# Performance work log

Measured on AMD Instinct MI355X. Metric: run time of the kernel, lower is better.

Reference implementation:

```python
import jax, jax.numpy as jnp
import numpy as np

D_MODEL = 1024
NUM_HEADS = 16
DEPTH = D_MODEL // NUM_HEADS


def setup_inputs() -> dict:
    key = jax.random.key(0)
    ks = jax.random.split(key, 9)
    s = 1.0 / np.sqrt(D_MODEL)
    x = jax.random.normal(ks[0], (2, 2048, D_MODEL), dtype=jnp.float32)
    def lin(kw, kb):
        W = jax.random.uniform(kw, (D_MODEL, D_MODEL), jnp.float32, -s, s)
        b = jax.random.uniform(kb, (D_MODEL,), jnp.float32, -s, s)
        return W, b
    Wq, bq = lin(ks[1], ks[2])
    Wk, bk = lin(ks[3], ks[4])
    Wv, bv = lin(ks[5], ks[6])
    Wo, bo = lin(ks[7], ks[8])
    return {"x": x, "Wq": Wq, "bq": bq, "Wk": Wk, "bk": bk,
            "Wv": Wv, "bv": bv, "Wo": Wo, "bo": bo}


def reference(x, Wq, bq, Wk, bk, Wv, bv, Wo, bo):
    B, T, _ = x.shape
    # projections; weights stored as [in, out] (torch Linear applies x @ W.T; here W is already [in,out])
    def split_heads(y):
        return y.reshape(B, T, NUM_HEADS, DEPTH).transpose(0, 2, 1, 3)  # [B,H,T,D]
    Q = split_heads(x @ Wq + bq)
    K = split_heads(x @ Wk + bk)
    V = split_heads(x @ Wv + bv)
    scale = 1.0 / jnp.sqrt(jnp.asarray(DEPTH, dtype=x.dtype))
    scores = jnp.einsum('bhqd,bhkd->bhqk', Q, K) * scale  # [B,H,T,T]
    attn = jax.nn.softmax(scores, axis=-1)
    out = jnp.einsum('bhqk,bhkd->bhqd', attn, V)  # [B,H,T,D]
    out = out.transpose(0, 2, 1, 3).reshape(B, T, D_MODEL)
    return out @ Wo + bo
```

## Files before the change

kernel.cpp:

```cpp
#include <hip/hip_runtime.h>
#include <hip/hip_bf16.h>

typedef unsigned short ushort_t;
typedef short s8v __attribute__((ext_vector_type(8)));
typedef float f4v __attribute__((ext_vector_type(4)));

#define DM 1024
#define TT 2048
#define NH 16
#define DH 64
#define QSCALE 0.18033688011112042f

__device__ __forceinline__ ushort_t f2bf(float f) {
  union { float f; unsigned u; } v; v.f = f;
  unsigned u = v.u;
  return (ushort_t)((u + 0x7fffu + ((u >> 16) & 1u)) >> 16);
}

__device__ __forceinline__ unsigned pk2bf(float a, float b) {
  union { __hip_bfloat162 h; unsigned u; } v;
  v.h = __float22bfloat162_rn(float2{a, b});
  return v.u;
}

__device__ __forceinline__ void gll16(const void* g, const void* l) {
  __builtin_amdgcn_global_load_lds(
      (const __attribute__((address_space(1))) unsigned int*)g,
      (__attribute__((address_space(3))) unsigned int*)l, 16, 0, 0);
}

__global__ __launch_bounds__(256) void wtrans4_kernel(const float* __restrict__ W0,
                                                      const float* __restrict__ W1,
                                                      const float* __restrict__ W2,
                                                      const float* __restrict__ W3,
                                                      ushort_t* __restrict__ dst) {
  __shared__ float tile[32][33];
  const int z = blockIdx.z;
  const float* W = z == 0 ? W0 : (z == 1 ? W1 : (z == 2 ? W2 : W3));
  ushort_t* Wt = dst + (size_t)z * DM * DM;
  int tx = threadIdx.x & 31, ty = threadIdx.x >> 5;
  int n0 = blockIdx.x * 32, k0 = blockIdx.y * 32;
#pragma unroll
  for (int i = 0; i < 4; i++)
    tile[ty + i * 8][tx] = W[(size_t)(k0 + ty + i * 8) * DM + n0 + tx];
  __syncthreads();
#pragma unroll
  for (int i = 0; i < 4; i++)
    Wt[(size_t)(n0 + ty + i * 8) * DM + k0 + tx] = f2bf(tile[tx][ty + i * 8]);
}

__global__ __launch_bounds__(256) void xconv_kernel(const float* __restrict__ x,
                                                    ushort_t* __restrict__ xb) {
  int i = blockIdx.x * 256 + threadIdx.x;
  const float4* p = (const float4*)x + (size_t)i * 2;
  float4 a = p[0], b = p[1];
  union { ushort_t s[8]; uint4 u; } r;
  r.s[0] = f2bf(a.x); r.s[1] = f2bf(a.y); r.s[2] = f2bf(a.z); r.s[3] = f2bf(a.w);
  r.s[4] = f2bf(b.x); r.s[5] = f2bf(b.y); r.s[6] = f2bf(b.z); r.s[7] = f2bf(b.w);
  *((uint4*)xb + i) = r.u;
}

__global__ __launch_bounds__(256) void vtrans_kernel(const ushort_t* __restrict__ V,
                                                     ushort_t* __restrict__ Vt) {
  __shared__ ushort_t Ls[64][72];
  const int t = threadIdx.x;
  const int t0 = blockIdx.x * 64, bh = blockIdx.y;
  const ushort_t* Vb = V + (size_t)bh * TT * DH;
  ushort_t* Vtb = Vt + (size_t)bh * DH * TT;
#pragma unroll
  for (int c = t; c < 512; c += 256) {
    int tt = c & 63, dch = c >> 6;
    union { uint4 u; ushort_t s[8]; } uu;
    uu.u = *(const uint4*)&Vb[(size_t)(t0 + tt) * DH + dch * 8];
#pragma unroll
    for (int i = 0; i < 8; i++) Ls[dch * 8 + i][tt] = uu.s[i];
  }
  __syncthreads();
#pragma unroll
  for (int c = t; c < 512; c += 256) {
    int d = c >> 3, tch = c & 7;
    uint4 u = *(const uint4*)&Ls[d][tch * 8];
    *(uint4*)&Vtb[(size_t)d * TT + t0 + tch * 8] = u;
  }
}

__global__ __launch_bounds__(256) void gemm_bt(
    const ushort_t* __restrict__ A, const ushort_t* __restrict__ Bt, int mode,
    const float* __restrict__ bias0, const float* __restrict__ bias1,
    const float* __restrict__ bias2,
    ushort_t* __restrict__ qo, ushort_t* __restrict__ ko, ushort_t* __restrict__ vo,
    float* __restrict__ co) {
  __shared__ __align__(16) ushort_t Asm[128 * 32];
  __shared__ __align__(16) ushort_t Bsm[128 * 32];
  const int m0 = blockIdx.x * 128, n0 = blockIdx.y * 128;
  const int t = threadIdx.x, lane = t & 63;
  const int wid = t >> 6, wr = wid >> 1, wc = wid & 1;
  const ushort_t* Ab = A + (size_t)m0 * DM;
  const ushort_t* Bb = Bt + (size_t)n0 * DM;

  f4v zero = {0.f, 0.f, 0.f, 0.f};
  f4v acc[4][4];
#pragma unroll
  for (int i = 0; i < 4; i++)
#pragma unroll
    for (int j = 0; j < 4; j++) acc[i][j] = zero;

  const int r0 = t >> 2;
  const int r1 = (t + 256) >> 2;
  const int k8a = (t & 3) * 8;
  const int rr = lane & 15, kk = (lane >> 4) * 8;

  for (int k0 = 0; k0 < DM; k0 += 32) {
    __syncthreads();
    gll16(Ab + (size_t)r0 * DM + k0 + k8a, &Asm[t * 8]);
    gll16(Ab + (size_t)r1 * DM + k0 + k8a, &Asm[(t + 256) * 8]);
    gll16(Bb + (size_t)r0 * DM + k0 + k8a, &Bsm[t * 8]);
    gll16(Bb + (size_t)r1 * DM + k0 + k8a, &Bsm[(t + 256) * 8]);
    asm volatile("s_waitcnt vmcnt(0)" ::: "memory");
    __syncthreads();

    s8v af[4], bf_[4];
#pragma unroll
    for (int mt = 0; mt < 4; mt++)
      af[mt] = *(const s8v*)&Asm[(wr * 64 + mt * 16 + rr) * 32 + kk];
#pragma unroll
    for (int nt = 0; nt < 4; nt++)
      bf_[nt] = *(const s8v*)&Bsm[(wc * 64 + nt * 16 + rr) * 32 + kk];
#pragma unroll
    for (int mt = 0; mt < 4; mt++)
#pragma unroll
      for (int nt = 0; nt < 4; nt++)
        acc[mt][nt] =
            __builtin_amdgcn_mfma_f32_16x16x32_bf16(af[mt], bf_[nt], acc[mt][nt], 0, 0, 0);
  }

  const int col_l = lane & 15, row_q = (lane >> 4) * 4;
  if (mode == 0) {
    const int qkv = n0 >> 10;
    const float* bias = qkv == 0 ? bias0 : (qkv == 1 ? bias1 : bias2);
    ushort_t* dst = qkv == 0 ? qo : (qkv == 1 ? ko : vo);
    const float sc = qkv == 0 ? QSCALE : 1.0f;
    const int nb = n0 & 1023;
#pragma unroll
    for (int nt = 0; nt < 4; nt++) {
      int gc = nb + wc * 64 + nt * 16 + col_l;
      float bv_ = bias[gc];
      int hh = gc >> 6, d = gc & 63;
#pragma unroll
      for (int mt = 0; mt < 4; mt++) {
#pragma unroll
        for (int j = 0; j < 4; j++) {
          int r = m0 + wr * 64 + mt * 16 + row_q + j;
          int bb = r >> 11, tt_ = r & 2047;
          dst[(((size_t)(bb * NH + hh)) * TT + tt_) * DH + d] = f2bf((acc[mt][nt][j] + bv_) * sc);
        }
      }
    }
  } else {
#pragma unroll
    for (int nt = 0; nt < 4; nt++) {
      int gc = n0 + wc * 64 + nt * 16 + col_l;
      float bv_ = bias0[gc];
#pragma unroll
      for (int mt = 0; mt < 4; mt++) {
#pragma unroll
        for (int j = 0; j < 4; j++) {
          int r = m0 + wr * 64 + mt * 16 + row_q + j;
          co[(size_t)r * DM + gc] = acc[mt][nt][j] + bv_;
        }
      }
    }
  }
}

__global__ __launch_bounds__(256) void attn_kernel(const ushort_t* __restrict__ Q,
                                                   const ushort_t* __restrict__ K,
                                                   const ushort_t* __restrict__ Vt,
                                                   ushort_t* __restrict__ O) {
  __shared__ __align__(16) ushort_t Ksm[64 * 64];
  __shared__ __align__(16) ushort_t Vsm[64 * 64];
  __shared__ __align__(16) ushort_t Psm[4][32 * 64];

  const int qt = blockIdx.x;
  const int bh = blockIdx.y;
  const int b = bh >> 4, h = bh & 15;
  const int t = threadIdx.x, lane = t & 63, wid = t >> 6;
  const ushort_t* Qb = Q + ((size_t)bh * TT + qt * 128) * DH;
  const ushort_t* Kb = K + (size_t)bh * TT * DH;
  const ushort_t* Vb = Vt + (size_t)bh * DH * TT;
  const int rr = lane & 15, quad = lane >> 4;
  const int rx = rr & 7;

  s8v qf[2][2];
#pragma unroll
  for (int mt = 0; mt < 2; mt++)
#pragma unroll
    for (int kh = 0; kh < 2; kh++)
      qf[mt][kh] = *(const s8v*)&Qb[(size_t)(wid * 32 + mt * 16 + rr) * DH + kh * 32 + quad * 8];

  f4v zero = {0.f, 0.f, 0.f, 0.f};
  f4v oacc[2][4];
  float mreg[2], lreg[2];
#pragma unroll
  for (int mt = 0; mt < 2; mt++) {
#pragma unroll
    for (int dt = 0; dt < 4; dt++) oacc[mt][dt] = zero;
    mreg[mt] = -1e30f;
    lreg[mt] = 0.f;
  }

  ushort_t* Pw = &Psm[wid][0];

  for (int kv0 = 0; kv0 < TT; kv0 += 64) {
    __syncthreads();
#pragma unroll
    for (int c = t; c < 512; c += 256) {
      int row = c >> 3;
      int sch = ((c & 7) ^ (row & 7)) * 8;
      gll16(&Kb[(size_t)(kv0 + row) * DH + sch], &Ksm[c * 8]);
      gll16(&Vb[(size_t)row * TT + kv0 + sch], &Vsm[c * 8]);
    }
    asm volatile("s_waitcnt vmcnt(0)" ::: "memory");
    __syncthreads();

    f4v st[2][4];
#pragma unroll
    for (int mt = 0; mt < 2; mt++)
#pragma unroll
      for (int ct = 0; ct < 4; ct++) st[mt][ct] = zero;
    __builtin_amdgcn_s_setprio(1);
#pragma unroll
    for (int ct = 0; ct < 4; ct++) {
      int key = ct * 16 + rr;
#pragma unroll
      for (int kh = 0; kh < 2; kh++) {
        s8v kf = *(const s8v*)&Ksm[key * 64 + (((kh * 4 + quad) ^ (key & 7)) << 3)];
#pragma unroll
        for (int mt = 0; mt < 2; mt++)
          st[mt][ct] = __builtin_amdgcn_mfma_f32_16x16x32_bf16(kf, qf[mt][kh], st[mt][ct], 0, 0, 0);
      }
    }
    __builtin_amdgcn_s_setprio(0);

#pragma unroll
    for (int mt = 0; mt < 2; mt++) {
      float a0 = fmaxf(fmaxf(st[mt][0][0], st[mt][0][1]), fmaxf(st[mt][0][2], st[mt][0][3]));
      float a1 = fmaxf(fmaxf(st[mt][1][0], st[mt][1][1]), fmaxf(st[mt][1][2], st[mt][1][3]));
      float a2 = fmaxf(fmaxf(st[mt][2][0], st[mt][2][1]), fmaxf(st[mt][2][2], st[mt][2][3]));
      float a3 = fmaxf(fmaxf(st[mt][3][0], st[mt][3][1]), fmaxf(st[mt][3][2], st[mt][3][3]));
      float pmax = fmaxf(fmaxf(a0, a1), fmaxf(a2, a3));
      pmax = fmaxf(pmax, __shfl_xor(pmax, 16, 64));
      pmax = fmaxf(pmax, __shfl_xor(pmax, 32, 64));
      float mold = mreg[mt];
      float mnew = fmaxf(mold, pmax);
      float corr = __builtin_amdgcn_exp2f(mold - mnew);
      mreg[mt] = mnew;
      float ps = 0.f;
#pragma unroll
      for (int ct = 0; ct < 4; ct++) {
#pragma unroll
        for (int j = 0; j < 4; j++) {
          float p = __builtin_amdgcn_exp2f(st[mt][ct][j] - mnew);
          st[mt][ct][j] = p;
          ps += p;
        }
      }
      ps += __shfl_xor(ps, 16, 64);
      ps += __shfl_xor(ps, 32, 64);
      lreg[mt] = lreg[mt] * corr + ps;
#pragma unroll
      for (int j = 0; j < 4; j++) {
        float cb = __shfl(corr, quad * 4 + j, 64);
#pragma unroll
        for (int dt = 0; dt < 4; dt++) oacc[mt][dt][j] *= cb;
      }
    }

#pragma unroll
    for (int mt = 0; mt < 2; mt++) {
#pragma unroll
      for (int ct = 0; ct < 4; ct++) {
        uint2 w;
        w.x = pk2bf(st[mt][ct][0], st[mt][ct][1]);
        w.y = pk2bf(st[mt][ct][2], st[mt][ct][3]);
        int chunk = 2 * ct + (quad >> 1);
        int idx = (mt * 16 + rr) * 64 + ((chunk ^ rx) << 3) + ((quad & 1) << 2);
        *(uint2*)&Pw[idx] = w;
      }
    }
    asm volatile("s_waitcnt lgkmcnt(0)" ::: "memory");
    __builtin_amdgcn_sched_barrier(0);

    __builtin_amdgcn_s_setprio(1);
#pragma unroll
    for (int mt = 0; mt < 2; mt++) {
#pragma unroll
      for (int kh2 = 0; kh2 < 2; kh2++) {
        s8v pa = *(const s8v*)&Pw[(mt * 16 + rr) * 64 + (((kh2 * 4 + quad) ^ rx) << 3)];
#pragma unroll
        for (int dt = 0; dt < 4; dt++) {
          int d = dt * 16 + rr;
          s8v vf = *(const s8v*)&Vsm[d * 64 + (((kh2 * 4 + quad) ^ rx) << 3)];
          oacc[mt][dt] = __builtin_amdgcn_mfma_f32_16x16x32_bf16(pa, vf, oacc[mt][dt], 0, 0, 0);
        }
      }
    }
    __builtin_amdgcn_s_setprio(0);
  }

#pragma unroll
  for (int mt = 0; mt < 2; mt++) {
    float linv = 1.0f / lreg[mt];
#pragma unroll
    for (int j = 0; j < 4; j++) {
      float lb = __shfl(linv, quad * 4 + j, 64);
      int row = qt * 128 + wid * 32 + mt * 16 + quad * 4 + j;
#pragma unroll
      for (int dt = 0; dt < 4; dt++) {
        int d = dt * 16 + rr;
        O[((size_t)(b * TT + row)) * DM + h * DH + d] = f2bf(oacc[mt][dt][j] * lb);
      }
    }
  }
}

extern "C" void kernel_launch(void* const* d_in, const int* in_sizes, int n_in,
                              void* d_out, int out_size, void* d_ws, size_t ws_size,
                              hipStream_t stream) {
  const float* x = (const float*)d_in[0];
  const float* Wq = (const float*)d_in[1];
  const float* bq = (const float*)d_in[2];
  const float* Wk = (const float*)d_in[3];
  const float* bk = (const float*)d_in[4];
  const float* Wv = (const float*)d_in[5];
  const float* bv = (const float*)d_in[6];
  const float* Wo = (const float*)d_in[7];
  const float* bo = (const float*)d_in[8];
  float* out = (float*)d_out;

  char* ws = (char*)d_ws;
  ushort_t* xb = (ushort_t*)(ws);
  ushort_t* wqkv = (ushort_t*)(ws + (8ull << 20));
  ushort_t* wot = (ushort_t*)(ws + (14ull << 20));
  ushort_t* Qb = (ushort_t*)(ws + (16ull << 20));
  ushort_t* Kb = (ushort_t*)(ws + (24ull << 20));
  ushort_t* Vb = (ushort_t*)(ws + (32ull << 20));
  ushort_t* Vtb = xb;
  ushort_t* Ob = Vb;

  dim3 tb(256);
  wtrans4_kernel<<<dim3(32, 32, 4), tb, 0, stream>>>(Wq, Wk, Wv, Wo, wqkv);
  xconv_kernel<<<dim3(2048), tb, 0, stream>>>(x, xb);
  gemm_bt<<<dim3(32, 24), tb, 0, stream>>>(xb, wqkv, 0, bq, bk, bv, Qb, Kb, Vb, nullptr);
  vtrans_kernel<<<dim3(32, 32), tb, 0, stream>>>(Vb, Vtb);
  attn_kernel<<<dim3(16, 32), tb, 0, stream>>>(Qb, Kb, Vtb, Ob);
  gemm_bt<<<dim3(32, 8), tb, 0, stream>>>(Ob, wot, 1, bo, nullptr, nullptr, nullptr, nullptr,
                                          nullptr, out);
}
```

Before: 240.3 us.

## Write V transposed from QKV GEMM, shrink attention tiles, add lazy softmax rescale

The QKV projection epilogue now writes V directly in [bh, d, t] layout, which removes the separate V transpose kernel and its extra memory round trip. The attention kernel uses 64-query blocks with one 16-row tile per wave, giving twice as many blocks and lower register use under a 4-waves occupancy hint. Blocks are remapped so that blocks sharing a head land on the same XCD for K/V cache reuse. Online softmax skips the rescale of the accumulator when the new max exceeds the old by no more than 8 (log2 units). In exchange, the V stores are strided, and each K/V tile now feeds less MFMA work per load.

```diff
diff --git a/kernel.cpp b/kernel.cpp
--- a/kernel.cpp
+++ b/kernel.cpp
@@ -58,30 +58,6 @@
   r.s[0] = f2bf(a.x); r.s[1] = f2bf(a.y); r.s[2] = f2bf(a.z); r.s[3] = f2bf(a.w);
   r.s[4] = f2bf(b.x); r.s[5] = f2bf(b.y); r.s[6] = f2bf(b.z); r.s[7] = f2bf(b.w);
   *((uint4*)xb + i) = r.u;
-}
-
-__global__ __launch_bounds__(256) void vtrans_kernel(const ushort_t* __restrict__ V,
-                                                     ushort_t* __restrict__ Vt) {
-  __shared__ ushort_t Ls[64][72];
-  const int t = threadIdx.x;
-  const int t0 = blockIdx.x * 64, bh = blockIdx.y;
-  const ushort_t* Vb = V + (size_t)bh * TT * DH;
-  ushort_t* Vtb = Vt + (size_t)bh * DH * TT;
-#pragma unroll
-  for (int c = t; c < 512; c += 256) {
-    int tt = c & 63, dch = c >> 6;
-    union { uint4 u; ushort_t s[8]; } uu;
-    uu.u = *(const uint4*)&Vb[(size_t)(t0 + tt) * DH + dch * 8];
-#pragma unroll
-    for (int i = 0; i < 8; i++) Ls[dch * 8 + i][tt] = uu.s[i];
-  }
-  __syncthreads();
-#pragma unroll
-  for (int c = t; c < 512; c += 256) {
-    int d = c >> 3, tch = c & 7;
-    uint4 u = *(const uint4*)&Ls[d][tch * 8];
-    *(uint4*)&Vtb[(size_t)d * TT + t0 + tch * 8] = u;
-  }
 }
 
 __global__ __launch_bounds__(256) void gemm_bt(
@@ -152,7 +128,13 @@
         for (int j = 0; j < 4; j++) {
           int r = m0 + wr * 64 + mt * 16 + row_q + j;
           int bb = r >> 11, tt_ = r & 2047;
-          dst[(((size_t)(bb * NH + hh)) * TT + tt_) * DH + d] = f2bf((acc[mt][nt][j] + bv_) * sc);
+          int bhh = bb * NH + hh;
+          ushort_t val = f2bf((acc[mt][nt][j] + bv_) * sc);
+          if (qkv == 2) {
+            dst[((size_t)bhh * DH + d) * TT + tt_] = val;
+          } else {
+            dst[((size_t)bhh * TT + tt_) * DH + d] = val;
+          }
         }
       }
     }
@@ -173,41 +155,37 @@
   }
 }
 
-__global__ __launch_bounds__(256) void attn_kernel(const ushort_t* __restrict__ Q,
-                                                   const ushort_t* __restrict__ K,
-                                                   const ushort_t* __restrict__ Vt,
-                                                   ushort_t* __restrict__ O) {
+__global__ __launch_bounds__(256, 4) void attn_kernel(const ushort_t* __restrict__ Q,
+                                                      const ushort_t* __restrict__ K,
+                                                      const ushort_t* __restrict__ Vt,
+                                                      ushort_t* __restrict__ O) {
   __shared__ __align__(16) ushort_t Ksm[64 * 64];
   __shared__ __align__(16) ushort_t Vsm[64 * 64];
-  __shared__ __align__(16) ushort_t Psm[4][32 * 64];
-
-  const int qt = blockIdx.x;
-  const int bh = blockIdx.y;
+  __shared__ __align__(16) ushort_t Psm[4][16 * 64];
+
+  const int b_lin = blockIdx.x + (blockIdx.y << 5);
+  const int xcd = b_lin & 7, n = b_lin >> 3;
+  const int bh = (xcd << 2) | (n >> 5);
+  const int qt = n & 31;
   const int b = bh >> 4, h = bh & 15;
   const int t = threadIdx.x, lane = t & 63, wid = t >> 6;
-  const ushort_t* Qb = Q + ((size_t)bh * TT + qt * 128) * DH;
+  const ushort_t* Qb = Q + ((size_t)bh * TT + qt * 64) * DH;
   const ushort_t* Kb = K + (size_t)bh * TT * DH;
   const ushort_t* Vb = Vt + (size_t)bh * DH * TT;
   const int rr = lane & 15, quad = lane >> 4;
   const int rx = rr & 7;
 
-  s8v qf[2][2];
-#pragma unroll
-  for (int mt = 0; mt < 2; mt++)
-#pragma unroll
-    for (int kh = 0; kh < 2; kh++)
-      qf[mt][kh] = *(const s8v*)&Qb[(size_t)(wid * 32 + mt * 16 + rr) * DH + kh * 32 + quad * 8];
+  s8v qf[2];
+#pragma unroll
+  for (int kh = 0; kh < 2; kh++)
+    qf[kh] = *(const s8v*)&Qb[(size_t)(wid * 16 + rr) * DH + kh * 32 + quad * 8];
 
   f4v zero = {0.f, 0.f, 0.f, 0.f};
-  f4v oacc[2][4];
-  float mreg[2], lreg[2];
-#pragma unroll
-  for (int mt = 0; mt < 2; mt++) {
-#pragma unroll
-    for (int dt = 0; dt < 4; dt++) oacc[mt][dt] = zero;
-    mreg[mt] = -1e30f;
-    lreg[mt] = 0.f;
-  }
+  f4v oacc[4];
+  float mreg = -1e30f;
+  float lreg = 0.f;
+#pragma unroll
+  for (int dt = 0; dt < 4; dt++) oacc[dt] = zero;
 
   ushort_t* Pw = &Psm[wid][0];
 
@@ -223,11 +201,9 @@
     asm volatile("s_waitcnt vmcnt(0)" ::: "memory");
     __syncthreads();
 
-    f4v st[2][4];
-#pragma unroll
-    for (int mt = 0; mt < 2; mt++)
-#pragma unroll
-      for (int ct = 0; ct < 4; ct++) st[mt][ct] = zero;
+    f4v st[4];
+#pragma unroll
+    for (int ct = 0; ct < 4; ct++) st[ct] = zero;
     __builtin_amdgcn_s_setprio(1);
 #pragma unroll
     for (int ct = 0; ct < 4; ct++) {
@@ -235,91 +211,84 @@
 #pragma unroll
       for (int kh = 0; kh < 2; kh++) {
         s8v kf = *(const s8v*)&Ksm[key * 64 + (((kh * 4 + quad) ^ (key & 7)) << 3)];
-#pragma unroll
-        for (int mt = 0; mt < 2; mt++)
-          st[mt][ct] = __builtin_amdgcn_mfma_f32_16x16x32_bf16(kf, qf[mt][kh], st[mt][ct], 0, 0, 0);
+        st[ct] = __builtin_amdgcn_mfma_f32_16x16x32_bf16(kf, qf[kh], st[ct], 0, 0, 0);
       }
     }
     __builtin_amdgcn_s_setprio(0);
 
-#pragma unroll
-    for (int mt = 0; mt < 2; mt++) {
-      float a0 = fmaxf(fmaxf(st[mt][0][0], st[mt][0][1]), fmaxf(st[mt][0][2], st[mt][0][3]));
-      float a1 = fmaxf(fmaxf(st[mt][1][0], st[mt][1][1]), fmaxf(st[mt][1][2], st[mt][1][3]));
-      float a2 = fmaxf(fmaxf(st[mt][2][0], st[mt][2][1]), fmaxf(st[mt][2][2], st[mt][2][3]));
-      float a3 = fmaxf(fmaxf(st[mt][3][0], st[mt][3][1]), fmaxf(st[mt][3][2], st[mt][3][3]));
-      float pmax = fmaxf(fmaxf(a0, a1), fmaxf(a2, a3));
-      pmax = fmaxf(pmax, __shfl_xor(pmax, 16, 64));
-      pmax = fmaxf(pmax, __shfl_xor(pmax, 32, 64));
-      float mold = mreg[mt];
-      float mnew = fmaxf(mold, pmax);
-      float corr = __builtin_amdgcn_exp2f(mold - mnew);
-      mreg[mt] = mnew;
-      float ps = 0.f;
-#pragma unroll
-      for (int ct = 0; ct < 4; ct++) {
-#pragma unroll
-        for (int j = 0; j < 4; j++) {
-          float p = __builtin_amdgcn_exp2f(st[mt][ct][j] - mnew);
-          st[mt][ct][j] = p;
-          ps += p;
-        }
-      }
-      ps += __shfl_xor(ps, 16, 64);
-      ps += __shfl_xor(ps, 32, 64);
-      lreg[mt] = lreg[mt] * corr + ps;
+    float a0 = fmaxf(fmaxf(st[0][0], st[0][1]), fmaxf(st[0][2], st[0][3]));
+    float a1 = fmaxf(fmaxf(st[1][0], st[1][1]), fmaxf(st[1][2], st[1][3]));
+    float a2 = fmaxf(fmaxf(st[2][0], st[2][1]), fmaxf(st[2][2], st[2][3]));
+    float a3 = fmaxf(fmaxf(st[3][0], st[3][1]), fmaxf(st[3][2], st[3][3]));
+    float pmax = fmaxf(fmaxf(a0, a1), fmaxf(a2, a3));
+    pmax = fmaxf(pmax, __shfl_xor(pmax, 16, 64));
+    pmax = fmaxf(pmax, __shfl_xor(pmax, 32, 64));
+    const bool rescale = !__all(pmax <= mreg + 8.0f);
+    float corr = 1.0f;
+    if (rescale) {
+      float mnew = fmaxf(mreg, pmax);
+      corr = __builtin_amdgcn_exp2f(mreg - mnew);
+      mreg = mnew;
+    }
+    float ps = 0.f;
+#pragma unroll
+    for (int ct = 0; ct < 4; ct++) {
+#pragma unroll
+      for (int j = 0; j < 4; j++) {
+        float p = __builtin_amdgcn_exp2f(st[ct][j] - mreg);
+        st[ct][j] = p;
+        ps += p;
+      }
+    }
+    ps += __shfl_xor(ps, 16, 64);
+    ps += __shfl_xor(ps, 32, 64);
+    if (rescale) {
+      lreg = lreg * corr + ps;
 #pragma unroll
       for (int j = 0; j < 4; j++) {
         float cb = __shfl(corr, quad * 4 + j, 64);
 #pragma unroll
-        for (int dt = 0; dt < 4; dt++) oacc[mt][dt][j] *= cb;
-      }
-    }
-
-#pragma unroll
-    for (int mt = 0; mt < 2; mt++) {
-#pragma unroll
-      for (int ct = 0; ct < 4; ct++) {
-        uint2 w;
-        w.x = pk2bf(st[mt][ct][0], st[mt][ct][1]);
-        w.y = pk2bf(st[mt][ct][2], st[mt][ct][3]);
-        int chunk = 2 * ct + (quad >> 1);
-        int idx = (mt * 16 + rr) * 64 + ((chunk ^ rx) << 3) + ((quad & 1) << 2);
-        *(uint2*)&Pw[idx] = w;
-      }
+        for (int dt = 0; dt < 4; dt++) oacc[dt][j] *= cb;
+      }
+    } else {
+      lreg += ps;
+    }
+
+#pragma unroll
+    for (int ct = 0; ct < 4; ct++) {
+      uint2 w;
+      w.x = pk2bf(st[ct][0], st[ct][1]);
+      w.y = pk2bf(st[ct][2], st[ct][3]);
+      int chunk = 2 * ct + (quad >> 1);
+      int idx = rr * 64 + ((chunk ^ rx) << 3) + ((quad & 1) << 2);
+      *(uint2*)&Pw[idx] = w;
     }
     asm volatile("s_waitcnt lgkmcnt(0)" ::: "memory");
     __builtin_amdgcn_sched_barrier(0);
 
     __builtin_amdgcn_s_setprio(1);
 #pragma unroll
-    for (int mt = 0; mt < 2; mt++) {
-#pragma unroll
-      for (int kh2 = 0; kh2 < 2; kh2++) {
-        s8v pa = *(const s8v*)&Pw[(mt * 16 + rr) * 64 + (((kh2 * 4 + quad) ^ rx) << 3)];
-#pragma unroll
-        for (int dt = 0; dt < 4; dt++) {
-          int d = dt * 16 + rr;
-          s8v vf = *(const s8v*)&Vsm[d * 64 + (((kh2 * 4 + quad) ^ rx) << 3)];
-          oacc[mt][dt] = __builtin_amdgcn_mfma_f32_16x16x32_bf16(pa, vf, oacc[mt][dt], 0, 0, 0);
-        }
+    for (int kh2 = 0; kh2 < 2; kh2++) {
+      s8v pa = *(const s8v*)&Pw[rr * 64 + (((kh2 * 4 + quad) ^ rx) << 3)];
+#pragma unroll
+      for (int dt = 0; dt < 4; dt++) {
+        int d = dt * 16 + rr;
+        s8v vf = *(const s8v*)&Vsm[d * 64 + (((kh2 * 4 + quad) ^ rx) << 3)];
+        oacc[dt] = __builtin_amdgcn_mfma_f32_16x16x32_bf16(pa, vf, oacc[dt], 0, 0, 0);
       }
     }
     __builtin_amdgcn_s_setprio(0);
   }
 
-#pragma unroll
-  for (int mt = 0; mt < 2; mt++) {
-    float linv = 1.0f / lreg[mt];
-#pragma unroll
-    for (int j = 0; j < 4; j++) {
-      float lb = __shfl(linv, quad * 4 + j, 64);
-      int row = qt * 128 + wid * 32 + mt * 16 + quad * 4 + j;
-#pragma unroll
-      for (int dt = 0; dt < 4; dt++) {
-        int d = dt * 16 + rr;
-        O[((size_t)(b * TT + row)) * DM + h * DH + d] = f2bf(oacc[mt][dt][j] * lb);
-      }
+  float linv = 1.0f / lreg;
+#pragma unroll
+  for (int j = 0; j < 4; j++) {
+    float lb = __shfl(linv, quad * 4 + j, 64);
+    int row = qt * 64 + wid * 16 + quad * 4 + j;
+#pragma unroll
+    for (int dt = 0; dt < 4; dt++) {
+      int d = dt * 16 + rr;
+      O[((size_t)(b * TT + row)) * DM + h * DH + d] = f2bf(oacc[dt][j] * lb);
     }
   }
 }
@@ -344,16 +313,14 @@
   ushort_t* wot = (ushort_t*)(ws + (14ull << 20));
   ushort_t* Qb = (ushort_t*)(ws + (16ull << 20));
   ushort_t* Kb = (ushort_t*)(ws + (24ull << 20));
-  ushort_t* Vb = (ushort_t*)(ws + (32ull << 20));
-  ushort_t* Vtb = xb;
-  ushort_t* Ob = Vb;
+  ushort_t* Vtb = (ushort_t*)(ws + (32ull << 20));
+  ushort_t* Ob = xb;
 
   dim3 tb(256);
   wtrans4_kernel<<<dim3(32, 32, 4), tb, 0, stream>>>(Wq, Wk, Wv, Wo, wqkv);
   xconv_kernel<<<dim3(2048), tb, 0, stream>>>(x, xb);
-  gemm_bt<<<dim3(32, 24), tb, 0, stream>>>(xb, wqkv, 0, bq, bk, bv, Qb, Kb, Vb, nullptr);
-  vtrans_kernel<<<dim3(32, 32), tb, 0, stream>>>(Vb, Vtb);
-  attn_kernel<<<dim3(16, 32), tb, 0, stream>>>(Qb, Kb, Vtb, Ob);
+  gemm_bt<<<dim3(32, 24), tb, 0, stream>>>(xb, wqkv, 0, bq, bk, bv, Qb, Kb, Vtb, nullptr);
+  attn_kernel<<<dim3(32, 32), tb, 0, stream>>>(Qb, Kb, Vtb, Ob);
   gemm_bt<<<dim3(32, 8), tb, 0, stream>>>(Ob, wot, 1, bo, nullptr, nullptr, nullptr, nullptr,
                                           nullptr, out);
 }
```

Measured after the change: 233.9 us. -2.7%, faster.
